# Performance work log

Measured on AMD Instinct MI355X. Metric: run time of the kernel, lower is better.

Reference implementation:

```python
import jax, jax.numpy as jnp
import numpy as np

BETA = 0.01

def quaternion_to_matrix(q):
    # q: (..., 4) real-part-first, not necessarily normalized
    r, i, j, k = q[..., 0], q[..., 1], q[..., 2], q[..., 3]
    two_s = 2.0 / jnp.sum(q * q, axis=-1)
    o = jnp.stack([
        1 - two_s * (j * j + k * k), two_s * (i * j - k * r), two_s * (i * k + j * r),
        two_s * (i * j + k * r), 1 - two_s * (i * i + k * k), two_s * (j * k - i * r),
        two_s * (i * k - j * r), two_s * (j * k + i * r), 1 - two_s * (i * i + j * j),
    ], axis=-1)
    return o.reshape(q.shape[:-1] + (3, 3))

def smooth_l1(x, target):
    d = jnp.abs(x - target)
    return jnp.where(d < BETA, 0.5 * d * d / BETA, d - 0.5 * BETA)

def setup_inputs() -> dict:
    key = jax.random.key(0)
    ks = jax.random.split(key, 5)
    b = 2097152
    return {
        "point_clouds": jax.random.normal(ks[0], (b, 3), dtype=jnp.float32),
        "target_transl": jax.random.normal(ks[1], (b, 3), dtype=jnp.float32),
        "target_rot": jax.random.normal(ks[2], (b, 4), dtype=jnp.float32),
        "transl_err": jax.random.normal(ks[3], (b, 3), dtype=jnp.float32),
        "rot_err": jax.random.normal(ks[4], (b, 4), dtype=jnp.float32),
    }

def reference(point_clouds, target_transl, target_rot, transl_err, rot_err):
    b = target_transl.shape[0]
    # pose_inverse: per-sample 3x3 inverse (vectorized, replaces the Python loop)
    R = quaternion_to_matrix(target_rot)                       # (b,3,3)
    R_inv = jnp.linalg.inv(R)                                  # (b,3,3)
    T_inv = -jnp.einsum('bij,bj->bi', R_inv, target_transl)    # (b,3)

    pred_r = quaternion_to_matrix(rot_err)                     # (b,3,3)
    pred_t = transl_err                                        # (b,3)

    # rotation loss against identity (flattened)
    r_mul = jnp.einsum('bij,bjk->bik', R_inv, pred_r).reshape(b, 9)
    eye9 = jnp.eye(3, dtype=r_mul.dtype).reshape(1, 9)
    loss_r = jnp.mean(jnp.sum(smooth_l1(r_mul, eye9), axis=1))

    # translation loss against zeros
    t_mul = jnp.einsum('bij,bj->bi', pred_r, T_inv) + pred_t   # (b,3)
    loss_t = jnp.mean(jnp.sum(smooth_l1(t_mul, 0.0), axis=1))

    total_loss = loss_r + loss_t
    return jnp.stack([total_loss, loss_t, loss_r])
```

## Files before the change

kernel.cpp:

```cpp
#include <hip/hip_runtime.h>

#define SL1_BETA 0.01f
#define NSLOT 256
#define CHUNK 256
#define BUFB  14336
#define LDS_BYTES (2 * BUFB)

#define AS1(p) ((const __attribute__((address_space(1))) void*)(p))
#define AS3(p) ((__attribute__((address_space(3))) void*)(p))

__device__ __forceinline__ float smooth_l1(float x) {
    float d = fabsf(x);
    return (d < SL1_BETA) ? (0.5f * d * d / SL1_BETA) : (d - 0.5f * SL1_BETA);
}

__device__ __forceinline__ void quat_to_mat9(float4 q, float R[9]) {
    float r = q.x, i = q.y, j = q.z, k = q.w;
    float two_s = 2.0f / (r*r + i*i + j*j + k*k);
    R[0] = 1.0f - two_s * (j*j + k*k);
    R[1] = two_s * (i*j - k*r);
    R[2] = two_s * (i*k + j*r);
    R[3] = two_s * (i*j + k*r);
    R[4] = 1.0f - two_s * (i*i + k*k);
    R[5] = two_s * (j*k - i*r);
    R[6] = two_s * (i*k - j*r);
    R[7] = two_s * (j*k + i*r);
    R[8] = 1.0f - two_s * (i*i + j*j);
}

__device__ __forceinline__ void sample_loss(float4 q, float4 e,
                                            float t0, float t1, float t2,
                                            float p0, float p1, float p2,
                                            float& sr, float& st) {
    float R[9], P[9];
    quat_to_mat9(q, R);
    quat_to_mat9(e, P);

    #pragma unroll
    for (int i2 = 0; i2 < 3; ++i2) {
        #pragma unroll
        for (int j2 = 0; j2 < 3; ++j2) {
            float v = R[0*3 + i2] * P[0*3 + j2]
                    + R[1*3 + i2] * P[1*3 + j2]
                    + R[2*3 + i2] * P[2*3 + j2];
            sr += smooth_l1(v - (i2 == j2 ? 1.0f : 0.0f));
        }
    }

    float Ti0 = -(R[0]*t0 + R[3]*t1 + R[6]*t2);
    float Ti1 = -(R[1]*t0 + R[4]*t1 + R[7]*t2);
    float Ti2 = -(R[2]*t0 + R[5]*t1 + R[8]*t2);

    st += smooth_l1(P[0]*Ti0 + P[1]*Ti1 + P[2]*Ti2 + p0);
    st += smooth_l1(P[3]*Ti0 + P[4]*Ti1 + P[5]*Ti2 + p1);
    st += smooth_l1(P[6]*Ti0 + P[7]*Ti1 + P[8]*Ti2 + p2);
}

__device__ __forceinline__ void stage_ops(
        const unsigned char* tq8, const unsigned char* qe8,
        const unsigned char* tt8, const unsigned char* te8,
        unsigned char* bufbase, long long s0, int wid, int lane) {
    #pragma unroll
    for (int u = 0; u < 4; ++u) {
        int o = wid + 4 * u;
        if (o < 14) {
            const unsigned char* src;
            if (o < 4)       src = tq8 + s0 * 16 + (size_t)o        * 1024;
            else if (o < 8)  src = qe8 + s0 * 16 + (size_t)(o - 4)  * 1024;
            else if (o < 11) src = tt8 + s0 * 12 + (size_t)(o - 8)  * 1024;
            else             src = te8 + s0 * 12 + (size_t)(o - 11) * 1024;
            __builtin_amdgcn_global_load_lds(AS1(src + (size_t)lane * 16),
                                             AS3(bufbase + (size_t)o * 1024),
                                             16, 0, 0);
        }
    }
}

__global__ __launch_bounds__(256, 5) void euler_loss_kernel(
        const float*  __restrict__ tt,
        const float4* __restrict__ tq,
        const float*  __restrict__ te,
        const float4* __restrict__ qe,
        double* __restrict__ acc, int b) {
    __shared__ __align__(16) unsigned char smem[LDS_BYTES];
    const int t    = threadIdx.x;
    const int lane = t & 63;
    const int wid  = t >> 6;

    const unsigned char* tq8 = (const unsigned char*)tq;
    const unsigned char* qe8 = (const unsigned char*)qe;
    const unsigned char* tt8 = (const unsigned char*)tt;
    const unsigned char* te8 = (const unsigned char*)te;

    float sr = 0.0f, st = 0.0f;

    long long nfull = (long long)b / CHUNK;
    long long c     = blockIdx.x;
    long long step  = gridDim.x;
    int cur = 0;
    bool have = (c < nfull);
    if (have) stage_ops(tq8, qe8, tt8, te8, smem, c * CHUNK, wid, lane);

    while (have) {
        long long cn = c + step;
        bool nhave = (cn < nfull);
        if (nhave)
            stage_ops(tq8, qe8, tt8, te8, smem + (cur ^ 1) * BUFB,
                      cn * CHUNK, wid, lane);
        if (nhave) {
            if (wid < 2) { asm volatile("s_waitcnt vmcnt(4)" ::: "memory"); }
            else         { asm volatile("s_waitcnt vmcnt(3)" ::: "memory"); }
        } else {
            asm volatile("s_waitcnt vmcnt(0)" ::: "memory");
        }
        __builtin_amdgcn_sched_barrier(0);
        __builtin_amdgcn_s_barrier();

        const unsigned char* bp = smem + cur * BUFB;
        const float4* tqL = (const float4*)(bp);
        const float4* qeL = (const float4*)(bp + 4096);
        const float*  ttL = (const float*) (bp + 8192);
        const float*  teL = (const float*) (bp + 11264);
        sample_loss(tqL[t], qeL[t],
                    ttL[3*t], ttL[3*t+1], ttL[3*t+2],
                    teL[3*t], teL[3*t+1], teL[3*t+2], sr, st);

        __builtin_amdgcn_s_barrier();
        cur ^= 1;
        c = cn;
        have = nhave;
    }

    for (long long s = nfull * CHUNK + (long long)blockIdx.x * blockDim.x + t;
         s < (long long)b; s += (long long)gridDim.x * blockDim.x) {
        sample_loss(tq[s], qe[s],
                    tt[3*s], tt[3*s+1], tt[3*s+2],
                    te[3*s], te[3*s+1], te[3*s+2], sr, st);
    }

    #pragma unroll
    for (int off = 32; off > 0; off >>= 1) {
        sr += __shfl_down(sr, off);
        st += __shfl_down(st, off);
    }
    if (lane == 0) {
        int slot = (blockIdx.x * 4 + wid) & (NSLOT - 1);
        double* sp = (double*)((unsigned char*)acc + (size_t)slot * 128);
        atomicAdd(&sp[0], (double)sr);
        atomicAdd(&sp[1], (double)st);
    }
}

__global__ __launch_bounds__(256) void euler_loss_finalize(
        const double* __restrict__ acc, float* __restrict__ out, int b) {
    int t = threadIdx.x;
    const double* sp = (const double*)((const unsigned char*)acc + (size_t)t * 128);
    double sr = sp[0], st = sp[1];
    #pragma unroll
    for (int off = 32; off > 0; off >>= 1) {
        sr += __shfl_down(sr, off);
        st += __shfl_down(st, off);
    }
    __shared__ double s_r[4], s_t[4];
    int lane = t & 63, wid = t >> 6;
    if (lane == 0) { s_r[wid] = sr; s_t[wid] = st; }
    __syncthreads();
    if (t == 0) {
        double tr  = s_r[0] + s_r[1] + s_r[2] + s_r[3];
        double tts = s_t[0] + s_t[1] + s_t[2] + s_t[3];
        double inv_b = 1.0 / (double)b;
        double lr = tr * inv_b;
        double lt = tts * inv_b;
        out[0] = (float)(lr + lt);
        out[1] = (float)lt;
        out[2] = (float)lr;
    }
}

extern "C" void kernel_launch(void* const* d_in, const int* in_sizes, int n_in,
                              void* d_out, int out_size, void* d_ws, size_t ws_size,
                              hipStream_t stream) {
    const float*  tt = (const float*)d_in[1];
    const float4* tq = (const float4*)d_in[2];
    const float*  te = (const float*)d_in[3];
    const float4* qe = (const float4*)d_in[4];
    float* out = (float*)d_out;
    int b = in_sizes[1] / 3;

    double* acc = (double*)d_ws;
    hipMemsetAsync(acc, 0, (size_t)NSLOT * 128, stream);

    long long nfull = (long long)b / CHUNK;
    int grid = 1280;
    if ((long long)grid > nfull) grid = (int)nfull;
    if (grid < 1) grid = 1;
    euler_loss_kernel<<<grid, 256, 0, stream>>>(tt, tq, te, qe, acc, b);
    euler_loss_finalize<<<1, 256, 0, stream>>>(acc, out, b);
}
```

Measured before the change: 35.41 us.

## Load quaternions directly to registers, stage only vec3 data via LDS

The two quaternion arrays, which are naturally coalesced as float4 per thread, now go straight into registers with a one-chunk-ahead software prefetch. Only the stride-3 translation arrays still pass through LDS via global_load_lds double buffering. This shrinks LDS per block from 28 KB to 12 KB, so occupancy is raised (launch bounds 8) and the grid grows to 2048 blocks. The loop now does its compute before waiting on the next loads, and it drops one barrier per iteration. The cost is more registers for the prefetched quaternions.

```diff
diff --git a/kernel.cpp b/kernel.cpp
--- a/kernel.cpp
+++ b/kernel.cpp
@@ -3,7 +3,7 @@
 #define SL1_BETA 0.01f
 #define NSLOT 256
 #define CHUNK 256
-#define BUFB  14336
+#define BUFB  6144
 #define LDS_BYTES (2 * BUFB)
 
 #define AS1(p) ((const __attribute__((address_space(1))) void*)(p))
@@ -56,19 +56,16 @@
     st += smooth_l1(P[6]*Ti0 + P[7]*Ti1 + P[8]*Ti2 + p2);
 }
 
-__device__ __forceinline__ void stage_ops(
-        const unsigned char* tq8, const unsigned char* qe8,
+__device__ __forceinline__ void stage_tt_te(
         const unsigned char* tt8, const unsigned char* te8,
         unsigned char* bufbase, long long s0, int wid, int lane) {
     #pragma unroll
-    for (int u = 0; u < 4; ++u) {
+    for (int u = 0; u < 2; ++u) {
         int o = wid + 4 * u;
-        if (o < 14) {
+        if (o < 6) {
             const unsigned char* src;
-            if (o < 4)       src = tq8 + s0 * 16 + (size_t)o        * 1024;
-            else if (o < 8)  src = qe8 + s0 * 16 + (size_t)(o - 4)  * 1024;
-            else if (o < 11) src = tt8 + s0 * 12 + (size_t)(o - 8)  * 1024;
-            else             src = te8 + s0 * 12 + (size_t)(o - 11) * 1024;
+            if (o < 3) src = tt8 + s0 * 12 + (size_t)o       * 1024;
+            else       src = te8 + s0 * 12 + (size_t)(o - 3) * 1024;
             __builtin_amdgcn_global_load_lds(AS1(src + (size_t)lane * 16),
                                              AS3(bufbase + (size_t)o * 1024),
                                              16, 0, 0);
@@ -76,7 +73,7 @@
     }
 }
 
-__global__ __launch_bounds__(256, 5) void euler_loss_kernel(
+__global__ __launch_bounds__(256, 8) void euler_loss_kernel(
         const float*  __restrict__ tt,
         const float4* __restrict__ tq,
         const float*  __restrict__ te,
@@ -87,53 +84,59 @@
     const int lane = t & 63;
     const int wid  = t >> 6;
 
-    const unsigned char* tq8 = (const unsigned char*)tq;
-    const unsigned char* qe8 = (const unsigned char*)qe;
     const unsigned char* tt8 = (const unsigned char*)tt;
     const unsigned char* te8 = (const unsigned char*)te;
 
     float sr = 0.0f, st = 0.0f;
 
-    long long nfull = (long long)b / CHUNK;
-    long long c     = blockIdx.x;
-    long long step  = gridDim.x;
+    const long long nfull = (long long)b / CHUNK;
+    long long c    = blockIdx.x;
+    const long long step = gridDim.x;
     int cur = 0;
     bool have = (c < nfull);
-    if (have) stage_ops(tq8, qe8, tt8, te8, smem, c * CHUNK, wid, lane);
+
+    float4 q, e;
+    if (have) {
+        stage_tt_te(tt8, te8, smem, c * CHUNK, wid, lane);
+        q = tq[c * CHUNK + t];
+        e = qe[c * CHUNK + t];
+        asm volatile("s_waitcnt vmcnt(0)" ::: "memory");
+    }
+    __builtin_amdgcn_s_barrier();
 
     while (have) {
         long long cn = c + step;
         bool nhave = (cn < nfull);
-        if (nhave)
-            stage_ops(tq8, qe8, tt8, te8, smem + (cur ^ 1) * BUFB,
-                      cn * CHUNK, wid, lane);
+        float4 qn, en;
         if (nhave) {
-            if (wid < 2) { asm volatile("s_waitcnt vmcnt(4)" ::: "memory"); }
-            else         { asm volatile("s_waitcnt vmcnt(3)" ::: "memory"); }
-        } else {
-            asm volatile("s_waitcnt vmcnt(0)" ::: "memory");
+            stage_tt_te(tt8, te8, smem + (cur ^ 1) * BUFB, cn * CHUNK, wid, lane);
+            qn = tq[cn * CHUNK + t];
+            en = qe[cn * CHUNK + t];
         }
+
+        const unsigned char* bp = smem + cur * BUFB;
+        const float*  ttL = (const float*)(bp);
+        const float*  teL = (const float*)(bp + 3072);
+        sample_loss(q, e,
+                    ttL[3*t], ttL[3*t+1], ttL[3*t+2],
+                    teL[3*t], teL[3*t+1], teL[3*t+2], sr, st);
+
+        asm volatile("s_waitcnt vmcnt(0)" ::: "memory");
         __builtin_amdgcn_sched_barrier(0);
         __builtin_amdgcn_s_barrier();
 
-        const unsigned char* bp = smem + cur * BUFB;
-        const float4* tqL = (const float4*)(bp);
-        const float4* qeL = (const float4*)(bp + 4096);
-        const float*  ttL = (const float*) (bp + 8192);
-        const float*  teL = (const float*) (bp + 11264);
-        sample_loss(tqL[t], qeL[t],
-                    ttL[3*t], ttL[3*t+1], ttL[3*t+2],
-                    teL[3*t], teL[3*t+1], teL[3*t+2], sr, st);
-
-        __builtin_amdgcn_s_barrier();
         cur ^= 1;
         c = cn;
+        q = qn;
+        e = en;
         have = nhave;
     }
 
+    const float4* tq4 = tq;
+    const float4* qe4 = qe;
     for (long long s = nfull * CHUNK + (long long)blockIdx.x * blockDim.x + t;
          s < (long long)b; s += (long long)gridDim.x * blockDim.x) {
-        sample_loss(tq[s], qe[s],
+        sample_loss(tq4[s], qe4[s],
                     tt[3*s], tt[3*s+1], tt[3*s+2],
                     te[3*s], te[3*s+1], te[3*s+2], sr, st);
     }
@@ -191,7 +194,7 @@
     hipMemsetAsync(acc, 0, (size_t)NSLOT * 128, stream);
 
     long long nfull = (long long)b / CHUNK;
-    int grid = 1280;
+    int grid = 2048;
     if ((long long)grid > nfull) grid = (int)nfull;
     if (grid < 1) grid = 1;
     euler_loss_kernel<<<grid, 256, 0, stream>>>(tt, tq, te, qe, acc, b);
```

Result: slower. 57.14 us (+61.4%).
